# Kernel tuning notes

Measured on AMD Instinct MI355X. Metric: run time of the kernel, lower is better.

Reference implementation:

```python
import jax, jax.numpy as jnp
import numpy as np

M = 100   # memory_size
D = 512   # memory_dim
B, C, H, W = 4, 512, 64, 64
LN_EPS = 512.0  # nn.LayerNorm(300, 512): 2nd positional arg is eps (faithful quirk)


def _l2norm(x):
    # F.normalize(x, dim=1): x / max(||x||_2, 1e-12)
    return x / jnp.maximum(jnp.linalg.norm(x, axis=1, keepdims=True), 1e-12)


def setup_inputs() -> dict:
    key = jax.random.key(0)
    ks = jax.random.split(key, 16)
    s = 0.03  # weight scale to keep activations sane
    return {
        "fea":    jax.random.normal(ks[0], (B, C, H, W), jnp.float32),
        "item_w": jax.random.normal(ks[1], (D, D), jnp.float32) * 0.02,
        "rel_w":  jax.random.normal(ks[2], (M, D, D), jnp.float32) * 0.02,
        "W1": jax.random.normal(ks[3], (C, D), jnp.float32) * s,  "b1": jnp.zeros((D,), jnp.float32),
        "W2": jax.random.normal(ks[4], (C, D), jnp.float32) * s,  "b2": jnp.zeros((D,), jnp.float32),
        "W3": jax.random.normal(ks[5], (C, M), jnp.float32) * s,  "b3": jnp.zeros((M,), jnp.float32),
        "Wqkv": jax.random.normal(ks[6], (D, 3 * M), jnp.float32) * s, "bqkv": jnp.zeros((3 * M,), jnp.float32),
        "ln_g": jnp.ones((3 * M,), jnp.float32), "ln_b": jnp.zeros((3 * M,), jnp.float32),
        "Wr1": jax.random.normal(ks[7], (D * D, D), jnp.float32) * s, "br1": jnp.zeros((D,), jnp.float32),
        "Wr2": jax.random.normal(ks[8], (M * D, D), jnp.float32) * s, "br2": jnp.zeros((D,), jnp.float32),
    }


def reference(fea, item_w, rel_w, W1, b1, W2, b2, W3, b3,
              Wqkv, bqkv, ln_g, ln_b, Wr1, br1, Wr2, br2):
    b, c, h, w = fea.shape
    x = fea.transpose(0, 2, 3, 1).reshape(b * h * w, c)        # (N, C)
    qn = _l2norm(x)
    ip1 = qn @ W1 + b1                                          # (N, D)
    ip2 = qn @ W2 + b2                                          # (N, D)
    ip3 = jax.nn.softmax(qn @ W3 + b3, axis=-1)                 # (N, M)
    # ip4[b,f] = sum_{n,d} ip3[b,n] ip2[b,d] rel_w[n,d,f]; scan over the M
    # memory slots to avoid an (N, M, D) intermediate.
    def _slot(acc, nw):
        coef, Wn = nw                                           # (N,), (D, D)
        return acc + coef[:, None] * (ip2 @ Wn), None
    ip4, _ = jax.lax.scan(_slot, jnp.zeros_like(ip2), (ip3.T, rel_w))
    # einsum('bd,cf->df', ip4, ip2) == outer(sum_b ip4, sum_c ip2)
    item0 = jnp.outer(ip4.sum(0), ip2.sum(0))                   # (D, D)
    item1 = item_w + ip1.T @ ip1                                # (D, D)
    qkv = (item0 + 1.0 * item1) @ Wqkv + bqkv                   # alpha2=1.0, (D, 3M)
    mu = qkv.mean(-1, keepdims=True)
    var = jnp.var(qkv, axis=-1, keepdims=True)                  # biased, as torch LN
    qkv = (qkv - mu) / jnp.sqrt(var + LN_EPS) * ln_g + ln_b
    q, k, v = qkv[:, :M].T, qkv[:, M:2 * M].T, qkv[:, 2 * M:].T  # each (M, D)
    # op_att: rel0[i,d,f] = sum_j tanh(q[i,d]*k[j,d]) * v[j,f]
    t = jnp.tanh(q[:, None, :] * k[None, :, :])                 # (M, M, D)
    rel0 = jnp.einsum('ijd,jf->idf', t, v)                      # (M, D, D)
    rel_w_new = rel_w + 1.0 * rel0                              # alpha1=1.0
    memory = rel_w_new.reshape(M, D * D) @ Wr1 + br1            # (M, D)
    mn = _l2norm(memory)
    addr = jax.nn.softmax(qn @ mn.T, axis=1)                    # (N, M)
    mf = (addr @ mn).reshape(b, h, w, c).transpose(0, 3, 1, 2)  # (b, C, h, w)
    return jnp.concatenate([fea, mf], axis=1)                   # (b, 2C, h, w)
```

## Files before the change

### kernel.cpp

```cpp
#include <hip/hip_runtime.h>
#include <hip/hip_bf16.h>

#define NTOK 16384
#define DDIM 512
#define MMEM 100
#define HWSZ 4096
#define QKVW 300

typedef __attribute__((ext_vector_type(8))) short short8v;
typedef __attribute__((ext_vector_type(4))) short short4v;
typedef __attribute__((ext_vector_type(4))) float f32x4;

__device__ __forceinline__ unsigned short f2bf(float x) {
  union { __hip_bfloat16 h; unsigned short u; } cv;
  cv.h = __float2bfloat16(x);
  return cv.u;
}
__device__ __forceinline__ float bf2f(unsigned short u) {
  union { unsigned int u; float f; } v; v.u = ((unsigned int)u) << 16;
  return v.f;
}

__global__ __launch_bounds__(256) void cvtw_k(
    const float* __restrict__ W1, const float* __restrict__ W2,
    const float* __restrict__ W3, const float* __restrict__ Wq,
    unsigned short* __restrict__ o1, unsigned short* __restrict__ o2,
    unsigned short* __restrict__ o3, unsigned short* __restrict__ oq) {
  int idx = blockIdx.x * 256 + threadIdx.x;
  const float* s; unsigned short* d; int off;
  if (idx < 262144)      { s = W1; d = o1; off = idx; }
  else if (idx < 524288) { s = W2; d = o2; off = idx - 262144; }
  else if (idx < 575488) { s = W3; d = o3; off = idx - 524288; }
  else if (idx < 729088) { s = Wq; d = oq; off = idx - 575488; }
  else return;
  d[off] = f2bf(s[off]);
}

__global__ __launch_bounds__(256) void feat_k(const float* __restrict__ fea,
                                              unsigned short* __restrict__ qnbf,
                                              float* __restrict__ out) {
  __shared__ float tile[512][33];
  __shared__ float psum[8][32];
  __shared__ float invn_s[32];
  const int bid = blockIdx.x;
  const int b = bid >> 7, hw0 = (bid & 127) * 32;
  const int t = threadIdx.x;
  const int hwo = t & 31, cg = t >> 5;
  const float* src = fea + (size_t)b * DDIM * HWSZ + hw0;
  float* dst = out + (size_t)b * (2 * DDIM) * HWSZ + hw0;
  float ss = 0.f;
#pragma unroll 8
  for (int i = 0; i < 64; ++i) {
    int c = cg * 64 + i;
    float v = src[(size_t)c * HWSZ + hwo];
    tile[c][hwo] = v;
    dst[(size_t)c * HWSZ + hwo] = v;
    ss += v * v;
  }
  psum[cg][hwo] = ss;
  __syncthreads();
  if (t < 32) {
    float s = 0.f;
#pragma unroll
    for (int j = 0; j < 8; ++j) s += psum[j][t];
    invn_s[t] = 1.f / fmaxf(sqrtf(s), 1e-12f);
  }
  __syncthreads();
  const int tok = t & 31, c0 = (t >> 5) * 64;
  const float inv = invn_s[tok];
  unsigned short* qp = qnbf + ((size_t)(b * HWSZ + hw0 + tok)) * DDIM + c0;
#pragma unroll
  for (int e8 = 0; e8 < 8; ++e8) {
    short8v p;
#pragma unroll
    for (int e = 0; e < 8; ++e)
      p[e] = (short)f2bf(tile[c0 + e8 * 8 + e][tok] * inv);
    *(short8v*)(qp + e8 * 8) = p;
  }
}

template<bool OUTBF>
__global__ __launch_bounds__(256) void gemm_bf16_k(
    const unsigned short* __restrict__ A, const unsigned short* __restrict__ B,
    const float* __restrict__ bias, void* __restrict__ Cv,
    int M, int N, int K, int lda, int ldb, int ldc) {
  __shared__ unsigned short As[128][40];
  __shared__ unsigned short Bs[32][132];
  const int tid = threadIdx.x;
  const int l = tid & 63, w = tid >> 6;
  const int l15 = l & 15, lhi = l >> 4;
  const int wm = w >> 1, wn = w & 1;
  const int row0 = blockIdx.y * 128, col0 = blockIdx.x * 128;
  const int am = tid >> 1, akq = (tid & 1) << 4;
  const int bk = tid >> 3, bnq = (tid & 7) << 4;
  const int arow = row0 + am;
  f32x4 acc[4][4] = {};

  for (int k0 = 0; k0 < K; k0 += 32) {
    short8v av0 = {}, av1 = {}, bv0 = {}, bv1 = {};
    if (arow < M && k0 + akq < K) {
      const unsigned short* ap = A + (size_t)arow * lda + k0 + akq;
      if (k0 + akq + 15 < K) {
        av0 = *(const short8v*)ap;
        av1 = *(const short8v*)(ap + 8);
      } else {
#pragma unroll
        for (int e = 0; e < 8; ++e) {
          av0[e] = (k0 + akq + e < K) ? (short)ap[e] : (short)0;
          av1[e] = (k0 + akq + 8 + e < K) ? (short)ap[8 + e] : (short)0;
        }
      }
    }
    {
      const int kk = k0 + bk;
      if (kk < K) {
        const unsigned short* bp = B + (size_t)kk * ldb + col0 + bnq;
        if (col0 + bnq + 15 < N) {
          bv0 = *(const short8v*)bp;
          bv1 = *(const short8v*)(bp + 8);
        } else {
#pragma unroll
          for (int e = 0; e < 8; ++e) {
            bv0[e] = (col0 + bnq + e < N) ? (short)bp[e] : (short)0;
            bv1[e] = (col0 + bnq + 8 + e < N) ? (short)bp[8 + e] : (short)0;
          }
        }
      }
    }
    __syncthreads();
    *(short8v*)&As[am][akq] = av0;
    *(short8v*)&As[am][akq + 8] = av1;
    *(short8v*)&Bs[bk][bnq] = bv0;
    *(short8v*)&Bs[bk][bnq + 8] = bv1;
    __syncthreads();
    short8v af[4];
#pragma unroll
    for (int mt = 0; mt < 4; ++mt)
      af[mt] = *(const short8v*)&As[wm * 64 + mt * 16 + l15][lhi * 8];
#pragma unroll
    for (int ct = 0; ct < 4; ++ct) {
      union { short8v v; unsigned short u[8]; } bf;
      const int nn = wn * 64 + ct * 16 + l15;
#pragma unroll
      for (int j = 0; j < 8; ++j) bf.u[j] = Bs[lhi * 8 + j][nn];
#pragma unroll
      for (int mt = 0; mt < 4; ++mt)
        acc[mt][ct] = __builtin_amdgcn_mfma_f32_16x16x32_bf16(
            af[mt], bf.v, acc[mt][ct], 0, 0, 0);
    }
  }

#pragma unroll
  for (int mt = 0; mt < 4; ++mt) {
    const int rb = row0 + wm * 64 + mt * 16 + lhi * 4;
#pragma unroll
    for (int u = 0; u < 4; ++u) {
      const int r = rb + u;
      if (r >= M) continue;
#pragma unroll
      for (int ct = 0; ct < 4; ++ct) {
        const int c = col0 + wn * 64 + ct * 16 + l15;
        if (c >= N) continue;
        float val = acc[mt][ct][u];
        if (bias) val += bias[c];
        if (OUTBF) ((unsigned short*)Cv)[(size_t)r * ldc + c] = f2bf(val);
        else       ((float*)Cv)[(size_t)r * ldc + c] = val;
      }
    }
  }
}

__global__ __launch_bounds__(256) void atb_bf16_k(
    const unsigned short* __restrict__ A, const unsigned short* __restrict__ B,
    float* __restrict__ C, int M, int N, int K,
    int lda, int ldb, int ldc, int KC) {
  __shared__ unsigned short As[128][40];
  __shared__ unsigned short Bs[32][132];
  const int tid = threadIdx.x;
  const int l = tid & 63, w = tid >> 6;
  const int l15 = l & 15, lhi = l >> 4;
  const int wm = w >> 1, wn = w & 1;
  const int row0 = blockIdx.y * 128, col0 = blockIdx.x * 128;
  const int kbeg = blockIdx.z * KC;
  const int kend = min(kbeg + KC, K);
  const int akk = tid >> 3, amq = (tid & 7) << 4;
  const int bk = tid >> 3, bnq = (tid & 7) << 4;
  f32x4 acc[4][4] = {};

  for (int k0 = kbeg; k0 < kend; k0 += 32) {
    unsigned short av[16]; short8v bv0 = {}, bv1 = {};
    {
      const int kk = k0 + akk;
      if (kk < kend) {
        const unsigned short* ap = A + (size_t)kk * lda + row0 + amq;
        if (row0 + amq + 15 < M) {
          *(short8v*)&av[0] = *(const short8v*)ap;
          *(short8v*)&av[8] = *(const short8v*)(ap + 8);
        } else {
#pragma unroll
          for (int e = 0; e < 16; ++e)
            av[e] = (row0 + amq + e < M) ? ap[e] : 0;
        }
      } else {
#pragma unroll
        for (int e = 0; e < 16; ++e) av[e] = 0;
      }
    }
    {
      const int kk = k0 + bk;
      if (kk < kend) {
        const unsigned short* bp = B + (size_t)kk * ldb + col0 + bnq;
        if (col0 + bnq + 15 < N) {
          bv0 = *(const short8v*)bp;
          bv1 = *(const short8v*)(bp + 8);
        } else {
#pragma unroll
          for (int e = 0; e < 8; ++e) {
            bv0[e] = (col0 + bnq + e < N) ? (short)bp[e] : (short)0;
            bv1[e] = (col0 + bnq + 8 + e < N) ? (short)bp[8 + e] : (short)0;
          }
        }
      }
    }
    __syncthreads();
#pragma unroll
    for (int e = 0; e < 16; ++e) As[amq + e][akk] = av[e];
    *(short8v*)&Bs[bk][bnq] = bv0;
    *(short8v*)&Bs[bk][bnq + 8] = bv1;
    __syncthreads();
    short8v af[4];
#pragma unroll
    for (int mt = 0; mt < 4; ++mt)
      af[mt] = *(const short8v*)&As[wm * 64 + mt * 16 + l15][lhi * 8];
#pragma unroll
    for (int ct = 0; ct < 4; ++ct) {
      union { short8v v; unsigned short u[8]; } bf;
      const int nn = wn * 64 + ct * 16 + l15;
#pragma unroll
      for (int j = 0; j < 8; ++j) bf.u[j] = Bs[lhi * 8 + j][nn];
#pragma unroll
      for (int mt = 0; mt < 4; ++mt)
        acc[mt][ct] = __builtin_amdgcn_mfma_f32_16x16x32_bf16(
            af[mt], bf.v, acc[mt][ct], 0, 0, 0);
    }
  }

#pragma unroll
  for (int mt = 0; mt < 4; ++mt) {
    const int rb = row0 + wm * 64 + mt * 16 + lhi * 4;
#pragma unroll
    for (int u = 0; u < 4; ++u) {
      const int r = rb + u;
      if (r >= M) continue;
#pragma unroll
      for (int ct = 0; ct < 4; ++ct) {
        const int c = col0 + wn * 64 + ct * 16 + l15;
        if (c >= N) continue;
        atomicAdd(&C[(size_t)r * ldc + c], acc[mt][ct][u]);
      }
    }
  }
}

__global__ __launch_bounds__(256) void rel0_mfma_k(
    const float* __restrict__ qm, const float* __restrict__ km,
    const float* __restrict__ vm, const float* __restrict__ rel_w,
    unsigned short* __restrict__ relbf) {
  __shared__ unsigned short Ts[128][136];
  __shared__ unsigned short Vs[128][136];
  __shared__ float qv[128];
  const int i = blockIdx.y;
  const int d0 = blockIdx.x * 128;
  const int tid = threadIdx.x;
  const int l = tid & 63, w = tid >> 6;
  const int l15 = l & 15, lhi = l >> 4;
  const int wm = w >> 1, wn = w & 1;

  if (tid < 128) qv[tid] = qm[(size_t)i * DDIM + d0 + tid];
  __syncthreads();
#pragma unroll
  for (int p = 0; p < 8; ++p) {
    int g = p * 2048 + tid * 8;
    int j = g >> 7, dd = g & 127;
    if (j < MMEM) {
      const float* kp = km + (size_t)j * DDIM + d0 + dd;
      float4 k0v = *(const float4*)kp;
      float4 k1v = *(const float4*)(kp + 4);
      float kv[8] = {k0v.x, k0v.y, k0v.z, k0v.w, k1v.x, k1v.y, k1v.z, k1v.w};
#pragma unroll
      for (int e = 0; e < 8; ++e)
        Ts[dd + e][j] = f2bf(tanhf(qv[dd + e] * kv[e]));
    } else {
#pragma unroll
      for (int e = 0; e < 8; ++e) Ts[dd + e][j] = 0;
    }
  }

  for (int f0 = 0; f0 < DDIM; f0 += 128) {
    __syncthreads();
#pragma unroll
    for (int p = 0; p < 8; ++p) {
      int g = p * 2048 + tid * 8;
      int j = g >> 7, ff = g & 127;
      short8v pv;
      if (j < MMEM) {
        const float* vp = vm + (size_t)j * DDIM + f0 + ff;
        float4 v0 = *(const float4*)vp;
        float4 v1 = *(const float4*)(vp + 4);
        pv[0] = (short)f2bf(v0.x); pv[1] = (short)f2bf(v0.y);
        pv[2] = (short)f2bf(v0.z); pv[3] = (short)f2bf(v0.w);
        pv[4] = (short)f2bf(v1.x); pv[5] = (short)f2bf(v1.y);
        pv[6] = (short)f2bf(v1.z); pv[7] = (short)f2bf(v1.w);
      } else {
#pragma unroll
        for (int e = 0; e < 8; ++e) pv[e] = 0;
      }
      *(short8v*)&Vs[j][ff] = pv;
    }
    __syncthreads();
    f32x4 acc[4][4] = {};
#pragma unroll
    for (int ks = 0; ks < 4; ++ks) {
      const int kb = ks * 32;
      short8v af[4];
#pragma unroll
      for (int mt = 0; mt < 4; ++mt)
        af[mt] = *(const short8v*)&Ts[wm * 64 + mt * 16 + l15][kb + lhi * 8];
#pragma unroll
      for (int ct = 0; ct < 4; ++ct) {
        union { short8v v; unsigned short u[8]; } bf;
        const int nn = wn * 64 + ct * 16 + l15;
#pragma unroll
        for (int jj = 0; jj < 8; ++jj) bf.u[jj] = Vs[kb + lhi * 8 + jj][nn];
#pragma unroll
        for (int mt = 0; mt < 4; ++mt)
          acc[mt][ct] = __builtin_amdgcn_mfma_f32_16x16x32_bf16(
              af[mt], bf.v, acc[mt][ct], 0, 0, 0);
      }
    }
#pragma unroll
    for (int mt = 0; mt < 4; ++mt) {
#pragma unroll
      for (int u = 0; u < 4; ++u) {
        const int d = d0 + wm * 64 + mt * 16 + lhi * 4 + u;
        const size_t base = (size_t)i * 262144 + (size_t)d * DDIM;
#pragma unroll
        for (int ct = 0; ct < 4; ++ct) {
          const int f = f0 + wn * 64 + ct * 16 + l15;
          relbf[base + f] = f2bf(rel_w[base + f] + acc[mt][ct][u]);
        }
      }
    }
  }
}

#define MGK 262144
#define MGKC 1024
#define MGCHUNK 256
__global__ __launch_bounds__(1024, 4) void memgemm_k(
    const unsigned short* __restrict__ Ag, const float* __restrict__ Bg,
    float* __restrict__ partial) {
  __shared__ unsigned short As[128][40];
  __shared__ unsigned short Bs[32][520];
  const int tid = threadIdx.x;
  const int l = tid & 63, w = tid >> 6;
  const int l15 = l & 15, lhi = l >> 4;
  const int kbeg = blockIdx.x * MGKC;
  const int arow = tid >> 3, akq = tid & 7;
  const int bk = tid >> 5, bnq = (tid & 31) * 16;
  f32x4 acc[8][2] = {};

  for (int t32 = 0; t32 < MGKC / 32; ++t32) {
    const int kb = kbeg + t32 * 32;
    short4v av = {};
    if (arow < MMEM)
      av = *(const short4v*)(Ag + (size_t)arow * MGK + kb + akq * 4);
    float4 bv[4];
    const float* bp = Bg + (size_t)(kb + bk) * DDIM + bnq;
#pragma unroll
    for (int u = 0; u < 4; ++u) bv[u] = *(const float4*)(bp + 4 * u);
    __syncthreads();
    *(short4v*)&As[arow][akq * 4] = av;
#pragma unroll
    for (int u = 0; u < 2; ++u) {
      short8v pb;
      pb[0] = (short)f2bf(bv[2*u].x);   pb[1] = (short)f2bf(bv[2*u].y);
      pb[2] = (short)f2bf(bv[2*u].z);   pb[3] = (short)f2bf(bv[2*u].w);
      pb[4] = (short)f2bf(bv[2*u+1].x); pb[5] = (short)f2bf(bv[2*u+1].y);
      pb[6] = (short)f2bf(bv[2*u+1].z); pb[7] = (short)f2bf(bv[2*u+1].w);
      *(short8v*)&Bs[bk][bnq + u * 8] = pb;
    }
    __syncthreads();
    union { short8v v; unsigned short u[8]; } bf0, bf1;
    const int nn0 = w * 32 + l15, nn1 = w * 32 + 16 + l15;
#pragma unroll
    for (int j = 0; j < 8; ++j) {
      bf0.u[j] = Bs[lhi * 8 + j][nn0];
      bf1.u[j] = Bs[lhi * 8 + j][nn1];
    }
#pragma unroll
    for (int mt = 0; mt < 8; ++mt) {
      short8v af = *(const short8v*)&As[mt * 16 + l15][lhi * 8];
      acc[mt][0] = __builtin_amdgcn_mfma_f32_16x16x32_bf16(af, bf0.v, acc[mt][0], 0, 0, 0);
      acc[mt][1] = __builtin_amdgcn_mfma_f32_16x16x32_bf16(af, bf1.v, acc[mt][1], 0, 0, 0);
    }
  }

  float* pw = partial + (size_t)blockIdx.x * (MMEM * DDIM);
#pragma unroll
  for (int mt = 0; mt < 8; ++mt) {
    const int r0 = mt * 16 + lhi * 4;
#pragma unroll
    for (int r = 0; r < 4; ++r) {
      const int row = r0 + r;
      if (row < MMEM) {
        pw[(size_t)row * DDIM + w * 32 + l15]      = acc[mt][0][r];
        pw[(size_t)row * DDIM + w * 32 + 16 + l15] = acc[mt][1][r];
      }
    }
  }
}

__global__ __launch_bounds__(512) void reduce_mn_k(
    const float* __restrict__ partial, const float* __restrict__ br1,
    unsigned short* __restrict__ mnbf, unsigned short* __restrict__ mnTbf) {
  __shared__ float r1[8];
  const int i = blockIdx.x, t = threadIdx.x;
  float a = br1[t];
  const float* p = partial + (size_t)i * DDIM + t;
  for (int z = 0; z < MGCHUNK; ++z) a += p[(size_t)z * (MMEM * DDIM)];
  float q = a * a;
#pragma unroll
  for (int o = 32; o; o >>= 1) q += __shfl_xor(q, o, 64);
  if ((t & 63) == 0) r1[t >> 6] = q;
  __syncthreads();
  q = 0.f;
#pragma unroll
  for (int j = 0; j < 8; ++j) q += r1[j];
  float inv = 1.f / fmaxf(sqrtf(q), 1e-12f);
  unsigned short hv = f2bf(a * inv);
  mnbf[(size_t)i * DDIM + t] = hv;
  mnTbf[(size_t)t * MMEM + i] = hv;
}

__global__ __launch_bounds__(256) void softmax_bf_k(const float* __restrict__ x,
                                                    unsigned short* __restrict__ o,
                                                    int nrows, int ldi, int ldo) {
  int wid = threadIdx.x >> 6;
  int lane = threadIdx.x & 63;
  int row = blockIdx.x * 4 + wid;
  if (row >= nrows) return;
  const float* xr = x + (size_t)row * ldi;
  float v0 = xr[lane];
  bool has1 = (lane + 64) < MMEM;
  float v1 = has1 ? xr[lane + 64] : -3.4e38f;
  float m = fmaxf(v0, v1);
#pragma unroll
  for (int off = 32; off; off >>= 1) m = fmaxf(m, __shfl_xor(m, off, 64));
  float e0 = expf(v0 - m);
  float e1 = has1 ? expf(v1 - m) : 0.f;
  float s = e0 + e1;
#pragma unroll
  for (int off = 32; off; off >>= 1) s += __shfl_xor(s, off, 64);
  float inv = 1.f / s;
  unsigned short* orow = o + (size_t)row * ldo;
  orow[lane] = f2bf(e0 * inv);
  if (has1) orow[lane + 64] = f2bf(e1 * inv);
}

__global__ __launch_bounds__(512) void colsum_bf_k(const unsigned short* __restrict__ A,
                                                   float* __restrict__ out) {
  int d = threadIdx.x;
  int r0 = blockIdx.x * 512;
  float a = 0.f;
  for (int r = 0; r < 512; ++r) a += bf2f(A[(size_t)(r0 + r) * DDIM + d]);
  atomicAdd(&out[d], a);
}

__global__ __launch_bounds__(256) void ip4sum_k(const float* __restrict__ S,
                                                const float* __restrict__ rel_w,
                                                float* __restrict__ out) {
  __shared__ float sv[128];
  int r0 = blockIdx.x * 128;
  int tid = threadIdx.x;
  if (tid < 128) sv[tid] = S[r0 + tid];
  __syncthreads();
  float a0 = 0.f, a1 = 0.f;
  for (int r = 0; r < 128; ++r) {
    const float* row = rel_w + (size_t)(r0 + r) * DDIM;
    float s = sv[r];
    a0 = fmaf(s, row[tid], a0);
    a1 = fmaf(s, row[tid + 256], a1);
  }
  atomicAdd(&out[tid], a0);
  atomicAdd(&out[tid + 256], a1);
}

__global__ __launch_bounds__(256) void assemble_item_k(
    const float* __restrict__ item, const float* __restrict__ item_w,
    const float* __restrict__ s4, const float* __restrict__ s2,
    unsigned short* __restrict__ itembf) {
  int idx = blockIdx.x * 256 + threadIdx.x;
  int d = idx >> 9, f = idx & 511;
  itembf[idx] = f2bf(item[idx] + item_w[idx] + s4[d] * s2[f]);
}

__global__ __launch_bounds__(256) void ln300_k(const float* __restrict__ x,
                                               const float* __restrict__ g,
                                               const float* __restrict__ bb,
                                               float* __restrict__ qm,
                                               float* __restrict__ km,
                                               float* __restrict__ vm) {
  __shared__ float r1[4], r2[4];
  int row = blockIdx.x, tid = threadIdx.x;
  const float* xr = x + (size_t)row * QKVW;
  float v1 = xr[tid];
  float v2 = (tid + 256 < QKVW) ? xr[tid + 256] : 0.f;
  float s = v1 + v2, q = v1 * v1 + v2 * v2;
#pragma unroll
  for (int o = 32; o; o >>= 1) { s += __shfl_xor(s, o, 64); q += __shfl_xor(q, o, 64); }
  if ((tid & 63) == 0) { r1[tid >> 6] = s; r2[tid >> 6] = q; }
  __syncthreads();
  s = r1[0] + r1[1] + r1[2] + r1[3];
  q = r2[0] + r2[1] + r2[2] + r2[3];
  float mean = s * (1.f / 300.f);
  float var = q * (1.f / 300.f) - mean * mean;
  float inv = rsqrtf(var + 512.0f);
  float y1 = (v1 - mean) * inv * g[tid] + bb[tid];
  int j = tid;
  if (j < 100)      qm[(size_t)j * DDIM + row] = y1;
  else if (j < 200) km[(size_t)(j - 100) * DDIM + row] = y1;
  else              vm[(size_t)(j - 200) * DDIM + row] = y1;
  if (tid + 256 < QKVW) {
    float y2 = (v2 - mean) * inv * g[tid + 256] + bb[tid + 256];
    vm[(size_t)(tid + 56) * DDIM + row] = y2;
  }
}

__global__ void write_mf_k(const float* __restrict__ mf, float* __restrict__ out) {
  __shared__ float tile[32][33];
  int b = blockIdx.z, hw0 = blockIdx.x * 32, c0 = blockIdx.y * 32;
  int tx = threadIdx.x, ty = threadIdx.y;
#pragma unroll
  for (int i = 0; i < 32; i += 8)
    tile[ty + i][tx] = mf[((size_t)b * HWSZ + hw0 + ty + i) * DDIM + c0 + tx];
  __syncthreads();
#pragma unroll
  for (int i = 0; i < 32; i += 8)
    out[(size_t)b * 4194304 + (size_t)(512 + c0 + ty + i) * HWSZ + hw0 + tx] =
        tile[tx][ty + i];
}

extern "C" void kernel_launch(void* const* d_in, const int* in_sizes, int n_in,
                              void* d_out, int out_size, void* d_ws, size_t ws_size,
                              hipStream_t stream) {
  (void)in_sizes; (void)n_in; (void)out_size; (void)ws_size;
  const float* fea    = (const float*)d_in[0];
  const float* item_w = (const float*)d_in[1];
  const float* rel_w  = (const float*)d_in[2];
  const float* W1     = (const float*)d_in[3];
  const float* W2     = (const float*)d_in[5];
  const float* W3     = (const float*)d_in[7];
  const float* b1     = (const float*)d_in[4];
  const float* b2     = (const float*)d_in[6];
  const float* b3     = (const float*)d_in[8];
  const float* Wqkv   = (const float*)d_in[9];
  const float* bqkv   = (const float*)d_in[10];
  const float* ln_g   = (const float*)d_in[11];
  const float* ln_b   = (const float*)d_in[12];
  const float* Wr1    = (const float*)d_in[13];
  const float* br1    = (const float*)d_in[14];
  float* out = (float*)d_out;
  float* ws = (float*)d_ws;

  float* ip3     = ws;
  float* addr    = ip3     + 1638400;
  float* mf      = addr    + 2097152;
  float* partial = mf      + 8388608;
  float* S       = partial + 13107200;
  float* ip4sum  = S       + 51200;
  float* ip2sum  = ip4sum  + 512;
  float* item    = ip2sum  + 512;
  float* qkv     = item    + 262144;
  float* qm      = qkv     + 153600;
  float* km      = qm      + 51200;
  float* vm      = km      + 51200;
  unsigned short* u16base = (unsigned short*)(vm + 51200);
  unsigned short* qnbf   = u16base;
  unsigned short* ip1bf  = qnbf   + 8388608;
  unsigned short* ip2bf  = ip1bf  + 8388608;
  unsigned short* ip3bf  = ip2bf  + 8388608;
  unsigned short* addrbf = ip3bf  + 1638400;
  unsigned short* relbf  = addrbf + 2097152;
  unsigned short* itembf = relbf  + 26214400;
  unsigned short* mnbf   = itembf + 262144;
  unsigned short* mnTbf  = mnbf   + 51200;
  unsigned short* W1bf   = mnTbf  + 51200;
  unsigned short* W2bf   = W1bf   + 262144;
  unsigned short* W3bf   = W2bf   + 262144;
  unsigned short* Wqbf   = W3bf   + 51200;

  hipMemsetAsync(S, 0, (size_t)(51200 + 512 + 512 + 262144) * sizeof(float), stream);

  cvtw_k<<<2848, 256, 0, stream>>>(W1, W2, W3, Wqkv, W1bf, W2bf, W3bf, Wqbf);

  feat_k<<<512, 256, 0, stream>>>(fea, qnbf, out);

  gemm_bf16_k<true><<<dim3(4, 128), 256, 0, stream>>>(
      qnbf, W1bf, b1, ip1bf, NTOK, DDIM, DDIM, DDIM, DDIM, DDIM);
  gemm_bf16_k<true><<<dim3(4, 128), 256, 0, stream>>>(
      qnbf, W2bf, b2, ip2bf, NTOK, DDIM, DDIM, DDIM, DDIM, DDIM);
  gemm_bf16_k<false><<<dim3(1, 128), 256, 0, stream>>>(
      qnbf, W3bf, b3, ip3, NTOK, MMEM, DDIM, DDIM, MMEM, MMEM);
  softmax_bf_k<<<4096, 256, 0, stream>>>(ip3, ip3bf, NTOK, MMEM, MMEM);

  atb_bf16_k<<<dim3(4, 4, 16), 256, 0, stream>>>(
      ip1bf, ip1bf, item, DDIM, DDIM, NTOK, DDIM, DDIM, DDIM, 1024);
  atb_bf16_k<<<dim3(4, 1, 16), 256, 0, stream>>>(
      ip3bf, ip2bf, S, MMEM, DDIM, NTOK, MMEM, DDIM, DDIM, 1024);
  colsum_bf_k<<<32, 512, 0, stream>>>(ip2bf, ip2sum);
  ip4sum_k<<<400, 256, 0, stream>>>(S, rel_w, ip4sum);

  assemble_item_k<<<1024, 256, 0, stream>>>(item, item_w, ip4sum, ip2sum, itembf);

  gemm_bf16_k<false><<<dim3(3, 4), 256, 0, stream>>>(
      itembf, Wqbf, bqkv, qkv, DDIM, QKVW, DDIM, DDIM, QKVW, QKVW);
  ln300_k<<<512, 256, 0, stream>>>(qkv, ln_g, ln_b, qm, km, vm);

  rel0_mfma_k<<<dim3(4, MMEM), 256, 0, stream>>>(qm, km, vm, rel_w, relbf);

  memgemm_k<<<dim3(MGCHUNK), 1024, 0, stream>>>(relbf, Wr1, partial);
  reduce_mn_k<<<MMEM, 512, 0, stream>>>(partial, br1, mnbf, mnTbf);

  gemm_bf16_k<false><<<dim3(1, 128), 256, 0, stream>>>(
      qnbf, mnTbf, nullptr, addr, NTOK, MMEM, DDIM, DDIM, MMEM, 128);
  softmax_bf_k<<<4096, 256, 0, stream>>>(addr, addrbf, NTOK, 128, 128);
  gemm_bf16_k<false><<<dim3(4, 128), 256, 0, stream>>>(
      addrbf, mnbf, nullptr, mf, NTOK, DDIM, MMEM, 128, DDIM, DDIM);

  write_mf_k<<<dim3(128, 16, 4), dim3(32, 8), 0, stream>>>(mf, out);
}
```

Baseline: 577.6 us.

## Fuse W1/W2 GEMMs, fuse softmax into GEMM, bf16 intermediates, vectorize feat

Concatenates W1 and W2 into one weight so ip1 and ip2 come from a single GEMM. Adds a GEMM kernel with the row softmax fused into its epilogue, replacing the separate fp32 logits write plus softmax pass for ip3 and addr. The memgemm partials and the mf intermediate are now stored in bf16, and memgemm uses twice as many, smaller K-chunks. feat_k switches to float4 loads and stores. The aim is to cut launches and HBM traffic, at the cost of extra rounding in the partial sums and in mf.

```diff
diff --git a/kernel.cpp b/kernel.cpp
--- a/kernel.cpp
+++ b/kernel.cpp
@@ -24,45 +24,53 @@
 __global__ __launch_bounds__(256) void cvtw_k(
     const float* __restrict__ W1, const float* __restrict__ W2,
     const float* __restrict__ W3, const float* __restrict__ Wq,
-    unsigned short* __restrict__ o1, unsigned short* __restrict__ o2,
-    unsigned short* __restrict__ o3, unsigned short* __restrict__ oq) {
+    const float* __restrict__ b1, const float* __restrict__ b2,
+    unsigned short* __restrict__ Wcat, unsigned short* __restrict__ o3,
+    unsigned short* __restrict__ oq, float* __restrict__ bcat) {
   int idx = blockIdx.x * 256 + threadIdx.x;
-  const float* s; unsigned short* d; int off;
-  if (idx < 262144)      { s = W1; d = o1; off = idx; }
-  else if (idx < 524288) { s = W2; d = o2; off = idx - 262144; }
-  else if (idx < 575488) { s = W3; d = o3; off = idx - 524288; }
-  else if (idx < 729088) { s = Wq; d = oq; off = idx - 575488; }
-  else return;
-  d[off] = f2bf(s[off]);
+  if (idx < 262144) {
+    int k = idx >> 9, n = idx & 511;
+    Wcat[(size_t)k * 1024 + n] = f2bf(W1[idx]);
+    Wcat[(size_t)k * 1024 + 512 + n] = f2bf(W2[idx]);
+  } else if (idx < 313344) {
+    o3[idx - 262144] = f2bf(W3[idx - 262144]);
+  } else if (idx < 466944) {
+    oq[idx - 313344] = f2bf(Wq[idx - 313344]);
+  } else if (idx < 467968) {
+    int i = idx - 466944;
+    bcat[i] = (i < 512) ? b1[i] : b2[i - 512];
+  }
 }
 
 __global__ __launch_bounds__(256) void feat_k(const float* __restrict__ fea,
                                               unsigned short* __restrict__ qnbf,
                                               float* __restrict__ out) {
-  __shared__ float tile[512][33];
-  __shared__ float psum[8][32];
+  __shared__ float tile[512][36];
+  __shared__ float psum[32][33];
   __shared__ float invn_s[32];
   const int bid = blockIdx.x;
   const int b = bid >> 7, hw0 = (bid & 127) * 32;
   const int t = threadIdx.x;
-  const int hwo = t & 31, cg = t >> 5;
-  const float* src = fea + (size_t)b * DDIM * HWSZ + hw0;
-  float* dst = out + (size_t)b * (2 * DDIM) * HWSZ + hw0;
-  float ss = 0.f;
-#pragma unroll 8
-  for (int i = 0; i < 64; ++i) {
-    int c = cg * 64 + i;
-    float v = src[(size_t)c * HWSZ + hwo];
-    tile[c][hwo] = v;
-    dst[(size_t)c * HWSZ + hwo] = v;
-    ss += v * v;
-  }
-  psum[cg][hwo] = ss;
+  const int hwq = t & 7, cg = t >> 3;
+  const float* src = fea + (size_t)b * DDIM * HWSZ + hw0 + hwq * 4;
+  float* dst = out + (size_t)b * (2 * DDIM) * HWSZ + hw0 + hwq * 4;
+  float ss[4] = {};
+#pragma unroll
+  for (int i = 0; i < 16; ++i) {
+    int c = cg * 16 + i;
+    float4 v = *(const float4*)(src + (size_t)c * HWSZ);
+    *(float4*)(dst + (size_t)c * HWSZ) = v;
+    *(float4*)&tile[c][hwq * 4] = v;
+    ss[0] += v.x * v.x; ss[1] += v.y * v.y;
+    ss[2] += v.z * v.z; ss[3] += v.w * v.w;
+  }
+#pragma unroll
+  for (int e = 0; e < 4; ++e) psum[hwq * 4 + e][cg] = ss[e];
   __syncthreads();
   if (t < 32) {
     float s = 0.f;
 #pragma unroll
-    for (int j = 0; j < 8; ++j) s += psum[j][t];
+    for (int j = 0; j < 32; ++j) s += psum[t][j];
     invn_s[t] = 1.f / fmaxf(sqrtf(s), 1e-12f);
   }
   __syncthreads();
@@ -170,6 +178,98 @@
   }
 }
 
+__global__ __launch_bounds__(256) void gemm_sm100_k(
+    const unsigned short* __restrict__ A, const unsigned short* __restrict__ B,
+    const float* __restrict__ bias, unsigned short* __restrict__ obf,
+    int lda, int ldb, int ldo) {
+  __shared__ unsigned short As[128][40];
+  __shared__ unsigned short Bs[32][132];
+  __shared__ float Ps[128][104];
+  const int tid = threadIdx.x;
+  const int l = tid & 63, w = tid >> 6;
+  const int l15 = l & 15, lhi = l >> 4;
+  const int wm = w >> 1, wn = w & 1;
+  const int row0 = blockIdx.x * 128;
+  const int am = tid >> 1, akq = (tid & 1) << 4;
+  const int bk = tid >> 3, bnq = (tid & 7) << 4;
+  f32x4 acc[4][4] = {};
+
+  for (int k0 = 0; k0 < DDIM; k0 += 32) {
+    const unsigned short* ap = A + (size_t)(row0 + am) * lda + k0 + akq;
+    short8v av0 = *(const short8v*)ap;
+    short8v av1 = *(const short8v*)(ap + 8);
+    short8v bv0 = {}, bv1 = {};
+    const unsigned short* bp = B + (size_t)(k0 + bk) * ldb + bnq;
+    if (bnq + 15 < MMEM) {
+      bv0 = *(const short8v*)bp;
+      bv1 = *(const short8v*)(bp + 8);
+    } else {
+#pragma unroll
+      for (int e = 0; e < 8; ++e) {
+        bv0[e] = (bnq + e < MMEM) ? (short)bp[e] : (short)0;
+        bv1[e] = (bnq + 8 + e < MMEM) ? (short)bp[8 + e] : (short)0;
+      }
+    }
+    __syncthreads();
+    *(short8v*)&As[am][akq] = av0;
+    *(short8v*)&As[am][akq + 8] = av1;
+    *(short8v*)&Bs[bk][bnq] = bv0;
+    *(short8v*)&Bs[bk][bnq + 8] = bv1;
+    __syncthreads();
+    short8v af[4];
+#pragma unroll
+    for (int mt = 0; mt < 4; ++mt)
+      af[mt] = *(const short8v*)&As[wm * 64 + mt * 16 + l15][lhi * 8];
+#pragma unroll
+    for (int ct = 0; ct < 4; ++ct) {
+      union { short8v v; unsigned short u[8]; } bf;
+      const int nn = wn * 64 + ct * 16 + l15;
+#pragma unroll
+      for (int j = 0; j < 8; ++j) bf.u[j] = Bs[lhi * 8 + j][nn];
+#pragma unroll
+      for (int mt = 0; mt < 4; ++mt)
+        acc[mt][ct] = __builtin_amdgcn_mfma_f32_16x16x32_bf16(
+            af[mt], bf.v, acc[mt][ct], 0, 0, 0);
+    }
+  }
+
+#pragma unroll
+  for (int mt = 0; mt < 4; ++mt) {
+#pragma unroll
+    for (int u = 0; u < 4; ++u) {
+      const int r = wm * 64 + mt * 16 + lhi * 4 + u;
+#pragma unroll
+      for (int ct = 0; ct < 4; ++ct) {
+        const int c = wn * 64 + ct * 16 + l15;
+        if (c < MMEM) {
+          float val = acc[mt][ct][u];
+          if (bias) val += bias[c];
+          Ps[r][c] = val;
+        }
+      }
+    }
+  }
+  __syncthreads();
+  for (int rr = 0; rr < 32; ++rr) {
+    const int r = w * 32 + rr;
+    float v0 = Ps[r][l];
+    const bool has1 = (l + 64) < MMEM;
+    float v1 = has1 ? Ps[r][l + 64] : -3.4e38f;
+    float m = fmaxf(v0, v1);
+#pragma unroll
+    for (int o = 32; o; o >>= 1) m = fmaxf(m, __shfl_xor(m, o, 64));
+    float e0 = expf(v0 - m);
+    float e1 = has1 ? expf(v1 - m) : 0.f;
+    float s = e0 + e1;
+#pragma unroll
+    for (int o = 32; o; o >>= 1) s += __shfl_xor(s, o, 64);
+    float inv = 1.f / s;
+    unsigned short* orow = obf + (size_t)(row0 + r) * ldo;
+    orow[l] = f2bf(e0 * inv);
+    if (has1) orow[l + 64] = f2bf(e1 * inv);
+  }
+}
+
 __global__ __launch_bounds__(256) void atb_bf16_k(
     const unsigned short* __restrict__ A, const unsigned short* __restrict__ B,
     float* __restrict__ C, int M, int N, int K,
@@ -355,11 +455,11 @@
 }
 
 #define MGK 262144
-#define MGKC 1024
-#define MGCHUNK 256
-__global__ __launch_bounds__(1024, 4) void memgemm_k(
+#define MGKC 512
+#define MGCHUNK 512
+__global__ __launch_bounds__(1024) void memgemm_k(
     const unsigned short* __restrict__ Ag, const float* __restrict__ Bg,
-    float* __restrict__ partial) {
+    unsigned short* __restrict__ partial) {
   __shared__ unsigned short As[128][40];
   __shared__ unsigned short Bs[32][520];
   const int tid = threadIdx.x;
@@ -406,7 +506,7 @@
     }
   }
 
-  float* pw = partial + (size_t)blockIdx.x * (MMEM * DDIM);
+  unsigned short* pw = partial + (size_t)blockIdx.x * (MMEM * DDIM);
 #pragma unroll
   for (int mt = 0; mt < 8; ++mt) {
     const int r0 = mt * 16 + lhi * 4;
@@ -414,21 +514,22 @@
     for (int r = 0; r < 4; ++r) {
       const int row = r0 + r;
       if (row < MMEM) {
-        pw[(size_t)row * DDIM + w * 32 + l15]      = acc[mt][0][r];
-        pw[(size_t)row * DDIM + w * 32 + 16 + l15] = acc[mt][1][r];
+        pw[(size_t)row * DDIM + w * 32 + l15]      = f2bf(acc[mt][0][r]);
+        pw[(size_t)row * DDIM + w * 32 + 16 + l15] = f2bf(acc[mt][1][r]);
       }
     }
   }
 }
 
 __global__ __launch_bounds__(512) void reduce_mn_k(
-    const float* __restrict__ partial, const float* __restrict__ br1,
+    const unsigned short* __restrict__ partial, const float* __restrict__ br1,
     unsigned short* __restrict__ mnbf, unsigned short* __restrict__ mnTbf) {
   __shared__ float r1[8];
   const int i = blockIdx.x, t = threadIdx.x;
   float a = br1[t];
-  const float* p = partial + (size_t)i * DDIM + t;
-  for (int z = 0; z < MGCHUNK; ++z) a += p[(size_t)z * (MMEM * DDIM)];
+  const unsigned short* p = partial + (size_t)i * DDIM + t;
+#pragma unroll 4
+  for (int z = 0; z < MGCHUNK; ++z) a += bf2f(p[(size_t)z * (MMEM * DDIM)]);
   float q = a * a;
 #pragma unroll
   for (int o = 32; o; o >>= 1) q += __shfl_xor(q, o, 64);
@@ -443,37 +544,12 @@
   mnTbf[(size_t)t * MMEM + i] = hv;
 }
 
-__global__ __launch_bounds__(256) void softmax_bf_k(const float* __restrict__ x,
-                                                    unsigned short* __restrict__ o,
-                                                    int nrows, int ldi, int ldo) {
-  int wid = threadIdx.x >> 6;
-  int lane = threadIdx.x & 63;
-  int row = blockIdx.x * 4 + wid;
-  if (row >= nrows) return;
-  const float* xr = x + (size_t)row * ldi;
-  float v0 = xr[lane];
-  bool has1 = (lane + 64) < MMEM;
-  float v1 = has1 ? xr[lane + 64] : -3.4e38f;
-  float m = fmaxf(v0, v1);
-#pragma unroll
-  for (int off = 32; off; off >>= 1) m = fmaxf(m, __shfl_xor(m, off, 64));
-  float e0 = expf(v0 - m);
-  float e1 = has1 ? expf(v1 - m) : 0.f;
-  float s = e0 + e1;
-#pragma unroll
-  for (int off = 32; off; off >>= 1) s += __shfl_xor(s, off, 64);
-  float inv = 1.f / s;
-  unsigned short* orow = o + (size_t)row * ldo;
-  orow[lane] = f2bf(e0 * inv);
-  if (has1) orow[lane + 64] = f2bf(e1 * inv);
-}
-
 __global__ __launch_bounds__(512) void colsum_bf_k(const unsigned short* __restrict__ A,
-                                                   float* __restrict__ out) {
+                                                   int ld, float* __restrict__ out) {
   int d = threadIdx.x;
   int r0 = blockIdx.x * 512;
   float a = 0.f;
-  for (int r = 0; r < 512; ++r) a += bf2f(A[(size_t)(r0 + r) * DDIM + d]);
+  for (int r = 0; r < 512; ++r) a += bf2f(A[(size_t)(r0 + r) * ld + d]);
   atomicAdd(&out[d], a);
 }
 
@@ -537,13 +613,15 @@
   }
 }
 
-__global__ void write_mf_k(const float* __restrict__ mf, float* __restrict__ out) {
+__global__ void write_mf_k(const unsigned short* __restrict__ mfbf,
+                           float* __restrict__ out) {
   __shared__ float tile[32][33];
   int b = blockIdx.z, hw0 = blockIdx.x * 32, c0 = blockIdx.y * 32;
   int tx = threadIdx.x, ty = threadIdx.y;
 #pragma unroll
   for (int i = 0; i < 32; i += 8)
-    tile[ty + i][tx] = mf[((size_t)b * HWSZ + hw0 + ty + i) * DDIM + c0 + tx];
+    tile[ty + i][tx] =
+        bf2f(mfbf[((size_t)b * HWSZ + hw0 + ty + i) * DDIM + c0 + tx]);
   __syncthreads();
 #pragma unroll
   for (int i = 0; i < 32; i += 8)
@@ -559,10 +637,10 @@
   const float* item_w = (const float*)d_in[1];
   const float* rel_w  = (const float*)d_in[2];
   const float* W1     = (const float*)d_in[3];
+  const float* b1     = (const float*)d_in[4];
   const float* W2     = (const float*)d_in[5];
+  const float* b2     = (const float*)d_in[6];
   const float* W3     = (const float*)d_in[7];
-  const float* b1     = (const float*)d_in[4];
-  const float* b2     = (const float*)d_in[6];
   const float* b3     = (const float*)d_in[8];
   const float* Wqkv   = (const float*)d_in[9];
   const float* bqkv   = (const float*)d_in[10];
@@ -573,11 +651,7 @@
   float* out = (float*)d_out;
   float* ws = (float*)d_ws;
 
-  float* ip3     = ws;
-  float* addr    = ip3     + 1638400;
-  float* mf      = addr    + 2097152;
-  float* partial = mf      + 8388608;
-  float* S       = partial + 13107200;
+  float* S       = ws;
   float* ip4sum  = S       + 51200;
   float* ip2sum  = ip4sum  + 512;
   float* item    = ip2sum  + 512;
@@ -585,40 +659,37 @@
   float* qm      = qkv     + 153600;
   float* km      = qm      + 51200;
   float* vm      = km      + 51200;
-  unsigned short* u16base = (unsigned short*)(vm + 51200);
-  unsigned short* qnbf   = u16base;
-  unsigned short* ip1bf  = qnbf   + 8388608;
-  unsigned short* ip2bf  = ip1bf  + 8388608;
-  unsigned short* ip3bf  = ip2bf  + 8388608;
-  unsigned short* addrbf = ip3bf  + 1638400;
-  unsigned short* relbf  = addrbf + 2097152;
-  unsigned short* itembf = relbf  + 26214400;
-  unsigned short* mnbf   = itembf + 262144;
-  unsigned short* mnTbf  = mnbf   + 51200;
-  unsigned short* W1bf   = mnTbf  + 51200;
-  unsigned short* W2bf   = W1bf   + 262144;
-  unsigned short* W3bf   = W2bf   + 262144;
-  unsigned short* Wqbf   = W3bf   + 51200;
+  float* bcat    = vm      + 51200;
+  unsigned short* u16base = (unsigned short*)(bcat + 1024);
+  unsigned short* qnbf    = u16base;
+  unsigned short* ip12bf  = qnbf    + 8388608;
+  unsigned short* ip3bf   = ip12bf  + 16777216;
+  unsigned short* addrbf  = ip3bf   + 1638400;
+  unsigned short* relbf   = addrbf  + 2097152;
+  unsigned short* partial = relbf   + 26214400;
+  unsigned short* mfbf    = partial + 26214400;
+  unsigned short* itembf  = mfbf    + 8388608;
+  unsigned short* mnbf    = itembf  + 262144;
+  unsigned short* mnTbf   = mnbf    + 51200;
+  unsigned short* Wcat    = mnTbf   + 51200;
+  unsigned short* W3bf    = Wcat    + 524288;
+  unsigned short* Wqbf    = W3bf    + 51200;
 
   hipMemsetAsync(S, 0, (size_t)(51200 + 512 + 512 + 262144) * sizeof(float), stream);
 
-  cvtw_k<<<2848, 256, 0, stream>>>(W1, W2, W3, Wqkv, W1bf, W2bf, W3bf, Wqbf);
+  cvtw_k<<<1828, 256, 0, stream>>>(W1, W2, W3, Wqkv, b1, b2, Wcat, W3bf, Wqbf, bcat);
 
   feat_k<<<512, 256, 0, stream>>>(fea, qnbf, out);
 
-  gemm_bf16_k<true><<<dim3(4, 128), 256, 0, stream>>>(
-      qnbf, W1bf, b1, ip1bf, NTOK, DDIM, DDIM, DDIM, DDIM, DDIM);
-  gemm_bf16_k<true><<<dim3(4, 128), 256, 0, stream>>>(
-      qnbf, W2bf, b2, ip2bf, NTOK, DDIM, DDIM, DDIM, DDIM, DDIM);
-  gemm_bf16_k<false><<<dim3(1, 128), 256, 0, stream>>>(
-      qnbf, W3bf, b3, ip3, NTOK, MMEM, DDIM, DDIM, MMEM, MMEM);
-  softmax_bf_k<<<4096, 256, 0, stream>>>(ip3, ip3bf, NTOK, MMEM, MMEM);
+  gemm_bf16_k<true><<<dim3(8, 128), 256, 0, stream>>>(
+      qnbf, Wcat, bcat, ip12bf, NTOK, 1024, DDIM, DDIM, 1024, 1024);
+  gemm_sm100_k<<<128, 256, 0, stream>>>(qnbf, W3bf, b3, ip3bf, DDIM, MMEM, MMEM);
 
   atb_bf16_k<<<dim3(4, 4, 16), 256, 0, stream>>>(
-      ip1bf, ip1bf, item, DDIM, DDIM, NTOK, DDIM, DDIM, DDIM, 1024);
+      ip12bf, ip12bf, item, DDIM, DDIM, NTOK, 1024, 1024, DDIM, 1024);
   atb_bf16_k<<<dim3(4, 1, 16), 256, 0, stream>>>(
-      ip3bf, ip2bf, S, MMEM, DDIM, NTOK, MMEM, DDIM, DDIM, 1024);
-  colsum_bf_k<<<32, 512, 0, stream>>>(ip2bf, ip2sum);
+      ip3bf, ip12bf + 512, S, MMEM, DDIM, NTOK, MMEM, 1024, DDIM, 1024);
+  colsum_bf_k<<<32, 512, 0, stream>>>(ip12bf + 512, 1024, ip2sum);
   ip4sum_k<<<400, 256, 0, stream>>>(S, rel_w, ip4sum);
 
   assemble_item_k<<<1024, 256, 0, stream>>>(item, item_w, ip4sum, ip2sum, itembf);
@@ -632,11 +703,9 @@
   memgemm_k<<<dim3(MGCHUNK), 1024, 0, stream>>>(relbf, Wr1, partial);
   reduce_mn_k<<<MMEM, 512, 0, stream>>>(partial, br1, mnbf, mnTbf);
 
-  gemm_bf16_k<false><<<dim3(1, 128), 256, 0, stream>>>(
-      qnbf, mnTbf, nullptr, addr, NTOK, MMEM, DDIM, DDIM, MMEM, 128);
-  softmax_bf_k<<<4096, 256, 0, stream>>>(addr, addrbf, NTOK, 128, 128);
-  gemm_bf16_k<false><<<dim3(4, 128), 256, 0, stream>>>(
-      addrbf, mnbf, nullptr, mf, NTOK, DDIM, MMEM, 128, DDIM, DDIM);
-
-  write_mf_k<<<dim3(128, 16, 4), dim3(32, 8), 0, stream>>>(mf, out);
-}
+  gemm_sm100_k<<<128, 256, 0, stream>>>(qnbf, mnTbf, nullptr, addrbf, DDIM, MMEM, 128);
+  gemm_bf16_k<true><<<dim3(4, 128), 256, 0, stream>>>(
+      addrbf, mnbf, nullptr, mfbf, NTOK, DDIM, MMEM, 128, DDIM, DDIM);
+
+  write_mf_k<<<dim3(128, 16, 4), dim3(32, 8), 0, stream>>>(mfbf, out);
+}
```

Measured after the change: 646.4 us. +11.9%, slower.
